# Performance work log

Measured on AMD Instinct MI355X. Metric: run time of the kernel, lower is better.

Reference implementation:

```python
import jax, jax.numpy as jnp
import numpy as np

LN_EPS = 1e-5

def _layernorm(x, gamma, beta):
    m = jnp.mean(x, axis=-1, keepdims=True)
    v = jnp.mean(jnp.square(x - m), axis=-1, keepdims=True)
    return (x - m) * jax.lax.rsqrt(v + LN_EPS) * gamma + beta

def setup_inputs() -> dict:
    N, D, B = 100000, 64, 512
    key = jax.random.key(0)
    k0, k1, k2, k3, k4, k5, k6 = jax.random.split(key, 7)
    query_place_ids = jax.random.randint(k0, (B,), 0, N)
    Eo = jax.random.normal(k1, (N, D), dtype=jnp.float32) * 0.02
    Ed = jax.random.normal(k2, (N, D), dtype=jnp.float32) * 0.02
    gamma_o = 1.0 + 0.01 * jax.random.normal(k3, (D,), dtype=jnp.float32)
    beta_o = 0.01 * jax.random.normal(k4, (D,), dtype=jnp.float32)
    gamma_d = 1.0 + 0.01 * jax.random.normal(k5, (D,), dtype=jnp.float32)
    beta_d = 0.01 * jax.random.normal(k6, (D,), dtype=jnp.float32)
    return {"query_place_ids": query_place_ids, "Eo": Eo, "Ed": Ed,
            "gamma_o": gamma_o, "beta_o": beta_o,
            "gamma_d": gamma_d, "beta_d": beta_d}

def reference(query_place_ids, Eo, Ed, gamma_o, beta_o, gamma_d, beta_d):
    # Dropout is inference-mode identity. LayerNorm is per-row, so
    # normalizing the full table then gathering equals gather-then-LN.
    # The torch expand()+bmm is mathematically a single shared GEMM
    # [B,D] x [D,N]; we express it that way (the fusion target).
    Co = _layernorm(Eo, gamma_o, beta_o)              # [N, D]
    Cd = _layernorm(Ed, gamma_d, beta_d)              # [N, D]
    q_out = Co[query_place_ids]                       # [B, D] (o-emb of queries)
    q_in = Cd[query_place_ids]                        # [B, D] (d-emb of queries)
    outflow_trans_weight = jax.nn.softmax(jnp.einsum('bd,nd->bn', q_out, Cd), axis=-1)
    inflow_trans_weight = jax.nn.softmax(jnp.einsum('bd,nd->bn', q_in, Co), axis=-1)
    return (outflow_trans_weight, inflow_trans_weight)
```

## Files before the change

kernel.cpp:

```cpp
#include <hip/hip_runtime.h>

typedef _Float16 half8 __attribute__((ext_vector_type(8)));
typedef float floatx4 __attribute__((ext_vector_type(4)));

#define DDIM 64
#define LN_EPS 1e-5f
#define SHIFT 20.0f

#define RB 128
#define CK 64
#define STR 72
#define ROWB (STR * 2)
#define PLB (CK * ROWB)
#define PSTR 68

__device__ inline float wave_sum(float v) {
#pragma unroll
  for (int m = 1; m < 64; m <<= 1) v += __shfl_xor(v, m, 64);
  return v;
}

__global__ __launch_bounds__(256) void ln_kernel(
    const float* __restrict__ Eo, const float* __restrict__ Ed,
    const float* __restrict__ go, const float* __restrict__ bo,
    const float* __restrict__ gd, const float* __restrict__ bd,
    _Float16* __restrict__ Co_hi, _Float16* __restrict__ Co_lo,
    _Float16* __restrict__ Cd_hi, _Float16* __restrict__ Cd_lo, int N) {
  int row = blockIdx.x * 4 + (threadIdx.x >> 6);
  if (row >= N) return;
  int lane = threadIdx.x & 63;
  size_t idx = (size_t)row * DDIM + lane;
  {
    float x = Eo[idx];
    float m = wave_sum(x) * (1.0f / DDIM);
    float d = x - m;
    float var = wave_sum(d * d) * (1.0f / DDIM);
    float y = d * rsqrtf(var + LN_EPS) * go[lane] + bo[lane];
    _Float16 hi = (_Float16)y;
    Co_hi[idx] = hi;
    Co_lo[idx] = (_Float16)(y - (float)hi);
  }
  {
    float x = Ed[idx];
    float m = wave_sum(x) * (1.0f / DDIM);
    float d = x - m;
    float var = wave_sum(d * d) * (1.0f / DDIM);
    float y = d * rsqrtf(var + LN_EPS) * gd[lane] + bd[lane];
    _Float16 hi = (_Float16)y;
    Cd_hi[idx] = hi;
    Cd_lo[idx] = (_Float16)(y - (float)hi);
  }
}

template <int PASS>
__global__ __launch_bounds__(256, 3) void score_kernel(
    const _Float16* __restrict__ Co_hi, const _Float16* __restrict__ Co_lo,
    const _Float16* __restrict__ Cd_hi, const _Float16* __restrict__ Cd_lo,
    const int* __restrict__ ids, float* __restrict__ sums,
    float* __restrict__ out, int N, int B, int nc_total) {
  __shared__ __attribute__((aligned(16))) char Sbuf[2 * PLB];
  __shared__ __attribute__((aligned(16))) float Pbuf[PASS == 1 ? RB * PSTR : 1];
  __shared__ float inv_lds[RB];

  const int t = threadIdx.x;
  const int mat = blockIdx.z;
  const int mbase = blockIdx.y * RB;
  const _Float16* Qsrc_h = (mat == 0) ? Co_hi : Cd_hi;
  const _Float16* Qsrc_l = (mat == 0) ? Co_lo : Cd_lo;
  const _Float16* Csrc_h = (mat == 0) ? Cd_hi : Co_hi;
  const _Float16* Csrc_l = (mat == 0) ? Cd_lo : Co_lo;

  const int lane = t & 63;
  const int wv = t >> 6;
  const int l15 = lane & 15;
  const int quad = lane >> 4;

  if (PASS == 1 && t < RB)
    inv_lds[t] = 1.0f / sums[(size_t)mat * B + mbase + t];

#pragma unroll
  for (int j = 0; j < 4; ++j) {
    int f = (j * 256 + t) * 16;
    int r = f >> 7;
    int off = f & 127;
    int id = ids[mbase + r];
    *(uint4*)(Sbuf + r * ROWB + off) =
        *(const uint4*)((const char*)Qsrc_h + (size_t)id * 128 + off);
  }
  __syncthreads();
  half8 Ah[2][2], Al[2][2];
#pragma unroll
  for (int mt = 0; mt < 2; ++mt) {
    int r = wv * 32 + mt * 16 + l15;
    const char* q = Sbuf + r * ROWB + quad * 16;
    Ah[mt][0] = *(const half8*)q;
    Ah[mt][1] = *(const half8*)(q + 64);
  }
  float invr[2][4];
  if (PASS == 1) {
#pragma unroll
    for (int mt = 0; mt < 2; ++mt)
#pragma unroll
      for (int r2 = 0; r2 < 4; ++r2)
        invr[mt][r2] = inv_lds[wv * 32 + mt * 16 + quad * 4 + r2];
  }
  __syncthreads();
#pragma unroll
  for (int j = 0; j < 4; ++j) {
    int f = (j * 256 + t) * 16;
    int r = f >> 7;
    int off = f & 127;
    int id = ids[mbase + r];
    *(uint4*)(Sbuf + r * ROWB + off) =
        *(const uint4*)((const char*)Qsrc_l + (size_t)id * 128 + off);
  }
  __syncthreads();
#pragma unroll
  for (int mt = 0; mt < 2; ++mt) {
    int r = wv * 32 + mt * 16 + l15;
    const char* q = Sbuf + r * ROWB + quad * 16;
    Al[mt][0] = *(const half8*)q;
    Al[mt][1] = *(const half8*)(q + 64);
  }
  __syncthreads();

  float sumacc[2][4];
#pragma unroll
  for (int mt = 0; mt < 2; ++mt)
#pragma unroll
    for (int r2 = 0; r2 < 4; ++r2) sumacc[mt][r2] = 0.0f;

  const int bx = blockIdx.x;
  const int gxd = gridDim.x;
  int nck = (bx < nc_total) ? ((nc_total - 1 - bx) / gxd + 1) : 0;
  float* orow = out + (size_t)mat * B * N + (size_t)mbase * N;

  for (int k = 0; k < nck; ++k) {
    int nbase = (bx + k * gxd) * CK;
#pragma unroll
    for (int p = 0; p < 2; ++p) {
      const char* src = (p == 0) ? (const char*)Csrc_h : (const char*)Csrc_l;
#pragma unroll
      for (int j = 0; j < 2; ++j) {
        int f = (j * 256 + t) * 16;
        int r = f >> 7;
        int off = f & 127;
        int gr = nbase + r;
        if (gr > N - 1) gr = N - 1;
        *(uint4*)(Sbuf + p * PLB + r * ROWB + off) =
            *(const uint4*)(src + (size_t)gr * 128 + off);
      }
    }
    __syncthreads();

#pragma unroll
    for (int nt = 0; nt < 4; ++nt) {
      int cr = nt * 16 + l15;
      const char* bh = Sbuf + cr * ROWB + quad * 16;
      const char* bl = bh + PLB;
      half8 Bh0 = *(const half8*)bh;
      half8 Bh1 = *(const half8*)(bh + 64);
      half8 Bl0 = *(const half8*)bl;
      half8 Bl1 = *(const half8*)(bl + 64);
      int col = nbase + nt * 16 + l15;
      bool valid = col < N;
#pragma unroll
      for (int mt = 0; mt < 2; ++mt) {
        floatx4 acc = {0.0f, 0.0f, 0.0f, 0.0f};
        acc = __builtin_amdgcn_mfma_f32_16x16x32_f16(Ah[mt][0], Bh0, acc, 0, 0, 0);
        acc = __builtin_amdgcn_mfma_f32_16x16x32_f16(Ah[mt][1], Bh1, acc, 0, 0, 0);
        acc = __builtin_amdgcn_mfma_f32_16x16x32_f16(Ah[mt][0], Bl0, acc, 0, 0, 0);
        acc = __builtin_amdgcn_mfma_f32_16x16x32_f16(Ah[mt][1], Bl1, acc, 0, 0, 0);
        acc = __builtin_amdgcn_mfma_f32_16x16x32_f16(Al[mt][0], Bh0, acc, 0, 0, 0);
        acc = __builtin_amdgcn_mfma_f32_16x16x32_f16(Al[mt][1], Bh1, acc, 0, 0, 0);
#pragma unroll
        for (int r2 = 0; r2 < 4; ++r2) {
          float p = __expf(acc[r2] - SHIFT);
          if (PASS == 0) {
            sumacc[mt][r2] += valid ? p : 0.0f;
          } else {
            int rl = wv * 32 + mt * 16 + quad * 4 + r2;
            Pbuf[rl * PSTR + nt * 16 + l15] = p * invr[mt][r2];
          }
        }
      }
    }
    if (PASS == 0) {
      __syncthreads();
    } else {
      __syncthreads();
#pragma unroll
      for (int i = 0; i < 8; ++i) {
        int fl = i * 256 + t;
        int row = fl >> 4;
        int c4 = fl & 15;
        int gcol = nbase + c4 * 4;
        if (gcol < N) {
          floatx4 v = *(const floatx4*)&Pbuf[row * PSTR + c4 * 4];
          __builtin_nontemporal_store(
              v, (floatx4*)(orow + (size_t)row * N + gcol));
        }
      }
    }
  }

  if (PASS == 0) {
#pragma unroll
    for (int mt = 0; mt < 2; ++mt)
#pragma unroll
      for (int r2 = 0; r2 < 4; ++r2) {
        float v = sumacc[mt][r2];
        v += __shfl_xor(v, 1, 64);
        v += __shfl_xor(v, 2, 64);
        v += __shfl_xor(v, 4, 64);
        v += __shfl_xor(v, 8, 64);
        if (l15 == 0) {
          int rl = wv * 32 + mt * 16 + quad * 4 + r2;
          atomicAdd(&sums[(size_t)mat * B + mbase + rl], v);
        }
      }
  }
}

extern "C" void kernel_launch(void* const* d_in, const int* in_sizes, int n_in,
                              void* d_out, int out_size, void* d_ws, size_t ws_size,
                              hipStream_t stream) {
  const int* ids = (const int*)d_in[0];
  const float* Eo = (const float*)d_in[1];
  const float* Ed = (const float*)d_in[2];
  const float* go = (const float*)d_in[3];
  const float* bo = (const float*)d_in[4];
  const float* gd = (const float*)d_in[5];
  const float* bd = (const float*)d_in[6];
  const int B = in_sizes[0];
  const int N = in_sizes[1] / DDIM;
  float* out = (float*)d_out;

  char* ws = (char*)d_ws;
  size_t plane = (size_t)N * DDIM * sizeof(_Float16);
  _Float16* Co_hi = (_Float16*)(ws + 0 * plane);
  _Float16* Co_lo = (_Float16*)(ws + 1 * plane);
  _Float16* Cd_hi = (_Float16*)(ws + 2 * plane);
  _Float16* Cd_lo = (_Float16*)(ws + 3 * plane);
  float* sums = (float*)(ws + 4 * plane);

  (void)hipMemsetAsync(sums, 0, (size_t)2 * B * sizeof(float), stream);

  ln_kernel<<<(N + 3) / 4, 256, 0, stream>>>(Eo, Ed, go, bo, gd, bd,
                                             Co_hi, Co_lo, Cd_hi, Cd_lo, N);

  int nc_total = (N + CK - 1) / CK;
  dim3 sgrid(96, B / RB, 2);
  score_kernel<0><<<sgrid, 256, 0, stream>>>(Co_hi, Co_lo, Cd_hi, Cd_lo, ids,
                                             sums, out, N, B, nc_total);
  score_kernel<1><<<sgrid, 256, 0, stream>>>(Co_hi, Co_lo, Cd_hi, Cd_lo, ids,
                                             sums, out, N, B, nc_total);
}
```

Measured before the change: 528.8 us.

## Split score passes, prefetch key tiles through registers, widen pass-0 chunk

Splits the templated score kernel into separate pass-0 (sum) and pass-1 (write) kernels. Both now prefetch the next key tile into registers while computing on the current LDS tile, so global latency overlaps with MFMA and exp work. Pass 0 widens its chunk to 128 rows, and both passes load the hi and lo query planes in one step, which removes extra barriers. Pass 1 reuses the Pbuf area to stage the lo query plane. The cost is higher register pressure from the staging arrays, which may reduce occupancy.

```diff
diff --git a/kernel.cpp b/kernel.cpp
--- a/kernel.cpp
+++ b/kernel.cpp
@@ -8,10 +8,11 @@
 #define SHIFT 20.0f
 
 #define RB 128
-#define CK 64
-#define STR 72
-#define ROWB (STR * 2)
-#define PLB (CK * ROWB)
+#define ROWB 144
+#define CK0 128
+#define CK1 64
+#define PLB0 (CK0 * ROWB)
+#define PLB1 (CK1 * ROWB)
 #define PSTR 68
 
 __device__ inline float wave_sum(float v) {
@@ -52,15 +53,12 @@
   }
 }
 
-template <int PASS>
-__global__ __launch_bounds__(256, 3) void score_kernel(
+__global__ __launch_bounds__(256, 3) void pass0_kernel(
     const _Float16* __restrict__ Co_hi, const _Float16* __restrict__ Co_lo,
     const _Float16* __restrict__ Cd_hi, const _Float16* __restrict__ Cd_lo,
     const int* __restrict__ ids, float* __restrict__ sums,
-    float* __restrict__ out, int N, int B, int nc_total) {
-  __shared__ __attribute__((aligned(16))) char Sbuf[2 * PLB];
-  __shared__ __attribute__((aligned(16))) float Pbuf[PASS == 1 ? RB * PSTR : 1];
-  __shared__ float inv_lds[RB];
+    int N, int B, int nc_total) {
+  __shared__ __attribute__((aligned(16))) char Sbuf[2 * PLB0];
 
   const int t = threadIdx.x;
   const int mat = blockIdx.z;
@@ -75,9 +73,6 @@
   const int l15 = lane & 15;
   const int quad = lane >> 4;
 
-  if (PASS == 1 && t < RB)
-    inv_lds[t] = 1.0f / sums[(size_t)mat * B + mbase + t];
-
 #pragma unroll
   for (int j = 0; j < 4; ++j) {
     int f = (j * 256 + t) * 16;
@@ -86,41 +81,19 @@
     int id = ids[mbase + r];
     *(uint4*)(Sbuf + r * ROWB + off) =
         *(const uint4*)((const char*)Qsrc_h + (size_t)id * 128 + off);
+    *(uint4*)(Sbuf + PLB0 + r * ROWB + off) =
+        *(const uint4*)((const char*)Qsrc_l + (size_t)id * 128 + off);
   }
   __syncthreads();
   half8 Ah[2][2], Al[2][2];
 #pragma unroll
   for (int mt = 0; mt < 2; ++mt) {
     int r = wv * 32 + mt * 16 + l15;
-    const char* q = Sbuf + r * ROWB + quad * 16;
-    Ah[mt][0] = *(const half8*)q;
-    Ah[mt][1] = *(const half8*)(q + 64);
-  }
-  float invr[2][4];
-  if (PASS == 1) {
-#pragma unroll
-    for (int mt = 0; mt < 2; ++mt)
-#pragma unroll
-      for (int r2 = 0; r2 < 4; ++r2)
-        invr[mt][r2] = inv_lds[wv * 32 + mt * 16 + quad * 4 + r2];
-  }
-  __syncthreads();
-#pragma unroll
-  for (int j = 0; j < 4; ++j) {
-    int f = (j * 256 + t) * 16;
-    int r = f >> 7;
-    int off = f & 127;
-    int id = ids[mbase + r];
-    *(uint4*)(Sbuf + r * ROWB + off) =
-        *(const uint4*)((const char*)Qsrc_l + (size_t)id * 128 + off);
-  }
-  __syncthreads();
-#pragma unroll
-  for (int mt = 0; mt < 2; ++mt) {
-    int r = wv * 32 + mt * 16 + l15;
-    const char* q = Sbuf + r * ROWB + quad * 16;
-    Al[mt][0] = *(const half8*)q;
-    Al[mt][1] = *(const half8*)(q + 64);
+    const char* qh = Sbuf + r * ROWB + quad * 16;
+    Ah[mt][0] = *(const half8*)qh;
+    Ah[mt][1] = *(const half8*)(qh + 64);
+    Al[mt][0] = *(const half8*)(qh + PLB0);
+    Al[mt][1] = *(const half8*)(qh + PLB0 + 64);
   }
   __syncthreads();
 
@@ -132,32 +105,45 @@
 
   const int bx = blockIdx.x;
   const int gxd = gridDim.x;
-  int nck = (bx < nc_total) ? ((nc_total - 1 - bx) / gxd + 1) : 0;
-  float* orow = out + (size_t)mat * B * N + (size_t)mbase * N;
-
+  int nck = (nc_total - 1 - bx) / gxd + 1;
+
+  uint4 stg[8];
+  auto load_regs = [&](int k) {
+    int nbase = (bx + k * gxd) * CK0;
+#pragma unroll
+    for (int u = 0; u < 8; ++u) {
+      int f = (u * 256 + t) * 16;
+      int p = f >> 14;
+      int fp = f & 16383;
+      int r = fp >> 7;
+      int off = fp & 127;
+      int gr = nbase + r;
+      if (gr > N - 1) gr = N - 1;
+      const char* src = (p == 0) ? (const char*)Csrc_h : (const char*)Csrc_l;
+      stg[u] = *(const uint4*)(src + (size_t)gr * 128 + off);
+    }
+  };
+
+  load_regs(0);
   for (int k = 0; k < nck; ++k) {
-    int nbase = (bx + k * gxd) * CK;
-#pragma unroll
-    for (int p = 0; p < 2; ++p) {
-      const char* src = (p == 0) ? (const char*)Csrc_h : (const char*)Csrc_l;
-#pragma unroll
-      for (int j = 0; j < 2; ++j) {
-        int f = (j * 256 + t) * 16;
-        int r = f >> 7;
-        int off = f & 127;
-        int gr = nbase + r;
-        if (gr > N - 1) gr = N - 1;
-        *(uint4*)(Sbuf + p * PLB + r * ROWB + off) =
-            *(const uint4*)(src + (size_t)gr * 128 + off);
-      }
+#pragma unroll
+    for (int u = 0; u < 8; ++u) {
+      int f = (u * 256 + t) * 16;
+      int p = f >> 14;
+      int fp = f & 16383;
+      int r = fp >> 7;
+      int off = fp & 127;
+      *(uint4*)(Sbuf + p * PLB0 + r * ROWB + off) = stg[u];
     }
     __syncthreads();
-
-#pragma unroll
-    for (int nt = 0; nt < 4; ++nt) {
+    if (k + 1 < nck) load_regs(k + 1);
+
+    int nbase = (bx + k * gxd) * CK0;
+#pragma unroll
+    for (int nt = 0; nt < 8; ++nt) {
       int cr = nt * 16 + l15;
       const char* bh = Sbuf + cr * ROWB + quad * 16;
-      const char* bl = bh + PLB;
+      const char* bl = bh + PLB0;
       half8 Bh0 = *(const half8*)bh;
       half8 Bh1 = *(const half8*)(bh + 64);
       half8 Bl0 = *(const half8*)bl;
@@ -176,49 +162,161 @@
 #pragma unroll
         for (int r2 = 0; r2 < 4; ++r2) {
           float p = __expf(acc[r2] - SHIFT);
-          if (PASS == 0) {
-            sumacc[mt][r2] += valid ? p : 0.0f;
-          } else {
-            int rl = wv * 32 + mt * 16 + quad * 4 + r2;
-            Pbuf[rl * PSTR + nt * 16 + l15] = p * invr[mt][r2];
-          }
+          sumacc[mt][r2] += valid ? p : 0.0f;
         }
       }
     }
-    if (PASS == 0) {
-      __syncthreads();
-    } else {
-      __syncthreads();
-#pragma unroll
-      for (int i = 0; i < 8; ++i) {
-        int fl = i * 256 + t;
-        int row = fl >> 4;
-        int c4 = fl & 15;
-        int gcol = nbase + c4 * 4;
-        if (gcol < N) {
-          floatx4 v = *(const floatx4*)&Pbuf[row * PSTR + c4 * 4];
-          __builtin_nontemporal_store(
-              v, (floatx4*)(orow + (size_t)row * N + gcol));
+    __syncthreads();
+  }
+
+#pragma unroll
+  for (int mt = 0; mt < 2; ++mt)
+#pragma unroll
+    for (int r2 = 0; r2 < 4; ++r2) {
+      float v = sumacc[mt][r2];
+      v += __shfl_xor(v, 1, 64);
+      v += __shfl_xor(v, 2, 64);
+      v += __shfl_xor(v, 4, 64);
+      v += __shfl_xor(v, 8, 64);
+      if (l15 == 0) {
+        int rl = wv * 32 + mt * 16 + quad * 4 + r2;
+        atomicAdd(&sums[(size_t)mat * B + mbase + rl], v);
+      }
+    }
+}
+
+__global__ __launch_bounds__(256, 3) void pass1_kernel(
+    const _Float16* __restrict__ Co_hi, const _Float16* __restrict__ Co_lo,
+    const _Float16* __restrict__ Cd_hi, const _Float16* __restrict__ Cd_lo,
+    const int* __restrict__ ids, const float* __restrict__ sums,
+    float* __restrict__ out, int N, int B, int nc_total) {
+  __shared__ __attribute__((aligned(16))) char Sbuf[2 * PLB1];
+  __shared__ __attribute__((aligned(16))) float Pbuf[RB * PSTR];
+  __shared__ float inv_lds[RB];
+
+  const int t = threadIdx.x;
+  const int mat = blockIdx.z;
+  const int mbase = blockIdx.y * RB;
+  const _Float16* Qsrc_h = (mat == 0) ? Co_hi : Cd_hi;
+  const _Float16* Qsrc_l = (mat == 0) ? Co_lo : Cd_lo;
+  const _Float16* Csrc_h = (mat == 0) ? Cd_hi : Co_hi;
+  const _Float16* Csrc_l = (mat == 0) ? Cd_lo : Co_lo;
+
+  const int lane = t & 63;
+  const int wv = t >> 6;
+  const int l15 = lane & 15;
+  const int quad = lane >> 4;
+
+  if (t < RB) inv_lds[t] = 1.0f / sums[(size_t)mat * B + mbase + t];
+
+  char* Qlo_area = (char*)Pbuf;
+#pragma unroll
+  for (int j = 0; j < 4; ++j) {
+    int f = (j * 256 + t) * 16;
+    int r = f >> 7;
+    int off = f & 127;
+    int id = ids[mbase + r];
+    *(uint4*)(Sbuf + r * ROWB + off) =
+        *(const uint4*)((const char*)Qsrc_h + (size_t)id * 128 + off);
+    *(uint4*)(Qlo_area + r * ROWB + off) =
+        *(const uint4*)((const char*)Qsrc_l + (size_t)id * 128 + off);
+  }
+  __syncthreads();
+  half8 Ah[2][2], Al[2][2];
+#pragma unroll
+  for (int mt = 0; mt < 2; ++mt) {
+    int r = wv * 32 + mt * 16 + l15;
+    const char* qh = Sbuf + r * ROWB + quad * 16;
+    const char* ql = Qlo_area + r * ROWB + quad * 16;
+    Ah[mt][0] = *(const half8*)qh;
+    Ah[mt][1] = *(const half8*)(qh + 64);
+    Al[mt][0] = *(const half8*)ql;
+    Al[mt][1] = *(const half8*)(ql + 64);
+  }
+  float invr[2][4];
+#pragma unroll
+  for (int mt = 0; mt < 2; ++mt)
+#pragma unroll
+    for (int r2 = 0; r2 < 4; ++r2)
+      invr[mt][r2] = inv_lds[wv * 32 + mt * 16 + quad * 4 + r2];
+  __syncthreads();
+
+  const int bx = blockIdx.x;
+  const int gxd = gridDim.x;
+  int nck = (nc_total - 1 - bx) / gxd + 1;
+  float* orow = out + (size_t)mat * B * N + (size_t)mbase * N;
+
+  uint4 stg[4];
+  auto load_regs = [&](int k) {
+    int nbase = (bx + k * gxd) * CK1;
+#pragma unroll
+    for (int u = 0; u < 4; ++u) {
+      int f = (u * 256 + t) * 16;
+      int p = f >> 13;
+      int fp = f & 8191;
+      int r = fp >> 7;
+      int off = fp & 127;
+      int gr = nbase + r;
+      if (gr > N - 1) gr = N - 1;
+      const char* src = (p == 0) ? (const char*)Csrc_h : (const char*)Csrc_l;
+      stg[u] = *(const uint4*)(src + (size_t)gr * 128 + off);
+    }
+  };
+
+  load_regs(0);
+  for (int k = 0; k < nck; ++k) {
+#pragma unroll
+    for (int u = 0; u < 4; ++u) {
+      int f = (u * 256 + t) * 16;
+      int p = f >> 13;
+      int fp = f & 8191;
+      int r = fp >> 7;
+      int off = fp & 127;
+      *(uint4*)(Sbuf + p * PLB1 + r * ROWB + off) = stg[u];
+    }
+    __syncthreads();
+    if (k + 1 < nck) load_regs(k + 1);
+
+    int nbase = (bx + k * gxd) * CK1;
+#pragma unroll
+    for (int nt = 0; nt < 4; ++nt) {
+      int cr = nt * 16 + l15;
+      const char* bh = Sbuf + cr * ROWB + quad * 16;
+      const char* bl = bh + PLB1;
+      half8 Bh0 = *(const half8*)bh;
+      half8 Bh1 = *(const half8*)(bh + 64);
+      half8 Bl0 = *(const half8*)bl;
+      half8 Bl1 = *(const half8*)(bl + 64);
+#pragma unroll
+      for (int mt = 0; mt < 2; ++mt) {
+        floatx4 acc = {0.0f, 0.0f, 0.0f, 0.0f};
+        acc = __builtin_amdgcn_mfma_f32_16x16x32_f16(Ah[mt][0], Bh0, acc, 0, 0, 0);
+        acc = __builtin_amdgcn_mfma_f32_16x16x32_f16(Ah[mt][1], Bh1, acc, 0, 0, 0);
+        acc = __builtin_amdgcn_mfma_f32_16x16x32_f16(Ah[mt][0], Bl0, acc, 0, 0, 0);
+        acc = __builtin_amdgcn_mfma_f32_16x16x32_f16(Ah[mt][1], Bl1, acc, 0, 0, 0);
+        acc = __builtin_amdgcn_mfma_f32_16x16x32_f16(Al[mt][0], Bh0, acc, 0, 0, 0);
+        acc = __builtin_amdgcn_mfma_f32_16x16x32_f16(Al[mt][1], Bh1, acc, 0, 0, 0);
+#pragma unroll
+        for (int r2 = 0; r2 < 4; ++r2) {
+          float p = __expf(acc[r2] - SHIFT);
+          int rl = wv * 32 + mt * 16 + quad * 4 + r2;
+          Pbuf[rl * PSTR + nt * 16 + l15] = p * invr[mt][r2];
         }
       }
     }
-  }
-
-  if (PASS == 0) {
-#pragma unroll
-    for (int mt = 0; mt < 2; ++mt)
-#pragma unroll
-      for (int r2 = 0; r2 < 4; ++r2) {
-        float v = sumacc[mt][r2];
-        v += __shfl_xor(v, 1, 64);
-        v += __shfl_xor(v, 2, 64);
-        v += __shfl_xor(v, 4, 64);
-        v += __shfl_xor(v, 8, 64);
-        if (l15 == 0) {
-          int rl = wv * 32 + mt * 16 + quad * 4 + r2;
-          atomicAdd(&sums[(size_t)mat * B + mbase + rl], v);
-        }
+    __syncthreads();
+
+#pragma unroll
+    for (int i = 0; i < 8; ++i) {
+      int fl = i * 256 + t;
+      int row = fl >> 4;
+      int c4 = fl & 15;
+      int gcol = nbase + c4 * 4;
+      if (gcol < N) {
+        floatx4 v = *(const floatx4*)&Pbuf[row * PSTR + c4 * 4];
+        __builtin_nontemporal_store(v, (floatx4*)(orow + (size_t)row * N + gcol));
       }
+    }
   }
 }
 
@@ -249,10 +347,11 @@
   ln_kernel<<<(N + 3) / 4, 256, 0, stream>>>(Eo, Ed, go, bo, gd, bd,
                                              Co_hi, Co_lo, Cd_hi, Cd_lo, N);
 
-  int nc_total = (N + CK - 1) / CK;
+  int nc0 = (N + CK0 - 1) / CK0;
+  int nc1 = (N + CK1 - 1) / CK1;
   dim3 sgrid(96, B / RB, 2);
-  score_kernel<0><<<sgrid, 256, 0, stream>>>(Co_hi, Co_lo, Cd_hi, Cd_lo, ids,
-                                             sums, out, N, B, nc_total);
-  score_kernel<1><<<sgrid, 256, 0, stream>>>(Co_hi, Co_lo, Cd_hi, Cd_lo, ids,
-                                             sums, out, N, B, nc_total);
-}
+  pass0_kernel<<<sgrid, 256, 0, stream>>>(Co_hi, Co_lo, Cd_hi, Cd_lo, ids,
+                                          sums, N, B, nc0);
+  pass1_kernel<<<sgrid, 256, 0, stream>>>(Co_hi, Co_lo, Cd_hi, Cd_lo, ids,
+                                          sums, out, N, B, nc1);
+}
```

Result: slower. 566.4 us (+7.1%).
